# Kernel tuning notes

Hardware: AMD Instinct MI355X
Metric: run time of the kernel (lower is better)

## Reference

```python
import jax, jax.numpy as jnp
import numpy as np

V, H, I, E, K, L = 32000, 1024, 4096, 8, 2, 2
B, S = 1, 2048

def setup_inputs() -> dict:
    key = jax.random.key(0)
    ks = jax.random.split(key, 8)
    s = 0.02
    d = {}
    d["input_ids"] = jax.random.randint(ks[0], (B, S), 0, V)
    d["emb"] = jax.random.normal(ks[1], (V, H), jnp.float32) * s
    d["router_w"] = jax.random.normal(ks[2], (L, E, H), jnp.float32) * s
    d["router_b"] = jnp.zeros((L, E), jnp.float32)
    d["fc1_w"] = jax.random.normal(ks[3], (L, E, I, H), jnp.float32) * s
    d["fc1_b"] = jnp.zeros((L, E, I), jnp.float32)
    d["fc2_w"] = jax.random.normal(ks[4], (L, E, H, I), jnp.float32) * s
    d["fc2_b"] = jnp.zeros((L, E, H), jnp.float32)
    d["ln_g"] = jnp.ones((L, H), jnp.float32)
    d["ln_b"] = jnp.zeros((L, H), jnp.float32)
    d["head_w"] = jax.random.normal(ks[5], (V, H), jnp.float32) * s
    d["head_b"] = jnp.zeros((V,), jnp.float32)
    return d

def _moe_layer(h, rw, rb, f1w, f1b, f2w, f2b, g, b):
    # h: [T,H]
    T = h.shape[0]
    logits = h @ rw.T + rb                                  # [T,E]
    top_w, sel = jax.lax.top_k(logits, K)                   # [T,K]
    top_w = jax.nn.softmax(top_w, axis=-1)
    sel_oh = sel[None, :, :] == jnp.arange(E)[:, None, None]  # [E,T,K]
    mask = sel_oh.any(-1)                                     # [E,T]
    w_tok = jnp.sum(jnp.where(sel_oh, top_w[None], 0.0), -1)  # [E,T]
    cnt = mask.sum(-1).astype(h.dtype)                        # [E]
    # faithful to source: per-expert SCALAR weight = mean of routing weights of routed tokens
    scal = jnp.where(cnt > 0, w_tok.sum(-1) / jnp.maximum(cnt, 1.0), 0.0)  # [E]
    a = jax.nn.gelu(jnp.einsum('th,eih->eti', h, f1w) + f1b[:, None, :], approximate=False)
    eo = jnp.einsum('eti,ehi->eth', a, f2w) + f2b[:, None, :]             # [E,T,H]
    out = jnp.einsum('et,eth->th', mask.astype(h.dtype) * scal[:, None], eo)
    mu = out.mean(-1, keepdims=True)
    var = out.var(-1, keepdims=True)
    out = (out - mu) / jnp.sqrt(var + 1e-5) * g + b
    counts = sel_oh.sum((1, 2)).astype(h.dtype)
    aux = jnp.mean((counts - T / E) ** 2) * 0.01
    return out, aux

def reference(input_ids, emb, router_w, router_b, fc1_w, fc1_b, fc2_w, fc2_b, ln_g, ln_b, head_w, head_b):
    h = emb[input_ids].reshape(-1, H)   # [T,H]
    aux_total = jnp.float32(0.0)
    for l in range(L):
        h, aux = _moe_layer(h, router_w[l], router_b[l], fc1_w[l], fc1_b[l],
                            fc2_w[l], fc2_b[l], ln_g[l], ln_b[l])
        aux_total = aux_total + aux
    logits = h @ head_w.T + head_b
    return logits.reshape(B, S, V), aux_total
```

## Files before the change

kernel.cpp:

```cpp
#include <hip/hip_runtime.h>
#include <math.h>

constexpr int kT = 2048;
constexpr int kH = 1024;
constexpr int kI = 4096;
constexpr int kE = 8;
constexpr int kV = 32000;
constexpr int kL = 2;
constexpr int kR = 4096;
constexpr int kSK = 4;
constexpr int kNB = kR / 128 + kE - 1;

typedef __attribute__((ext_vector_type(4))) float f32x4;
typedef __attribute__((ext_vector_type(8))) short bf16x8;

__device__ inline unsigned cvtpk(float lo, float hi) {
  unsigned r;
  asm("v_cvt_pk_bf16_f32 %0, %1, %2" : "=v"(r) : "v"(lo), "v"(hi));
  return r;
}

__device__ inline unsigned short f2bf(float x) {
  union { float f; unsigned u; } c; c.f = x;
  unsigned u = c.u;
  u += 0x7FFFu + ((u >> 16) & 1u);
  return (unsigned short)(u >> 16);
}

__device__ inline void dec2(float x, float y,
                            unsigned& p1, unsigned& p2, unsigned& p3) {
  unsigned ux = __float_as_uint(x), uy = __float_as_uint(y);
  unsigned x1 = ux & 0xFFFF0000u, y1 = uy & 0xFFFF0000u;
  float rx = x - __uint_as_float(x1), ry = y - __uint_as_float(y1);
  unsigned x2 = __float_as_uint(rx) & 0xFFFF0000u;
  unsigned y2 = __float_as_uint(ry) & 0xFFFF0000u;
  float sx = rx - __uint_as_float(x2), sy = ry - __uint_as_float(y2);
  p1 = (x1 >> 16) | y1;
  p2 = (x2 >> 16) | y2;
  p3 = (__float_as_uint(sx) >> 16) | (__float_as_uint(sy) & 0xFFFF0000u);
}

__device__ inline int swz(int e) { return e ^ (((e >> 6) & 3) << 3); }


__global__ void gather_k(const int* __restrict__ ids, const float* __restrict__ emb,
                         float* __restrict__ h) {
  int t = blockIdx.x;
  int id = ids[t];
  const float4* src = (const float4*)(emb + (size_t)id * kH);
  float4* dst = (float4*)(h + (size_t)t * kH);
  dst[threadIdx.x] = src[threadIdx.x];
}

__global__ void router_k(const float* __restrict__ h, const float* __restrict__ rw,
                         const float* __restrict__ rb, float* __restrict__ logits) {
  int t = blockIdx.x;
  int lg = threadIdx.x & 31;
  int e = threadIdx.x >> 5;
  const float* hr = h + (size_t)t * kH;
  const float* wr = rw + (size_t)e * kH;
  float p = 0.f;
  for (int k = lg * 4; k < kH; k += 128) {
    float4 a = *(const float4*)(hr + k);
    float4 b = *(const float4*)(wr + k);
    p += a.x * b.x + a.y * b.y + a.z * b.z + a.w * b.w;
  }
  for (int o = 16; o > 0; o >>= 1) p += __shfl_down(p, o, 32);
  if (lg == 0) logits[t * kE + e] = p + rb[e];
}

__global__ void topk_k(const float* __restrict__ logits, int* __restrict__ sel,
                       float* __restrict__ w_sum, int* __restrict__ cnt) {
  int t = blockIdx.x * blockDim.x + threadIdx.x;
  if (t >= kT) return;
  float v[8];
#pragma unroll
  for (int e = 0; e < 8; e++) v[e] = logits[t * 8 + e];
  int e1 = 0; float v1 = v[0];
#pragma unroll
  for (int e = 1; e < 8; e++) if (v[e] > v1) { v1 = v[e]; e1 = e; }
  int e2 = -1; float v2 = -3.4e38f;
#pragma unroll
  for (int e = 0; e < 8; e++) if (e != e1 && v[e] > v2) { v2 = v[e]; e2 = e; }
  float z = expf(v2 - v1);
  float w1 = 1.f / (1.f + z);
  float w2 = z * w1;
  sel[t * 2] = e1;
  sel[t * 2 + 1] = e2;
  atomicAdd(&w_sum[e1], w1);
  atomicAdd(&w_sum[e2], w2);
  atomicAdd(&cnt[e1], 1);
  atomicAdd(&cnt[e2], 1);
}

__global__ void finalize_k(const int* __restrict__ cnt, const float* __restrict__ w_sum,
                           float* __restrict__ scal, int* __restrict__ off,
                           int* __restrict__ fill, float* __restrict__ aux,
                           int* __restrict__ blk_e, int* __restrict__ blk_m) {
  if (threadIdx.x == 0) {
    int o = 0;
    float a = 0.f;
    for (int e = 0; e < 8; e++) {
      off[e] = o;
      o += cnt[e];
      fill[e] = 0;
      int c = cnt[e];
      scal[e] = c > 0 ? w_sum[e] / (float)c : 0.f;
      float d = (float)c - 256.f;
      a += d * d;
    }
    aux[0] += 0.01f * (a * 0.125f);
    int nb = 0;
    for (int e = 0; e < 8; e++)
      for (int m = 0; m < cnt[e]; m += 128) { blk_e[nb] = e; blk_m[nb] = m; nb++; }
    for (int i = nb; i < kNB; i++) { blk_e[i] = -1; blk_m[i] = 0; }
  }
}

__global__ void scatter_k(const int* __restrict__ sel, const int* __restrict__ off,
                          int* __restrict__ fill, int* __restrict__ list,
                          int* __restrict__ pos) {
  int t = blockIdx.x * blockDim.x + threadIdx.x;
  if (t >= kT) return;
#pragma unroll
  for (int s = 0; s < 2; s++) {
    int e = sel[t * 2 + s];
    int p = atomicAdd(&fill[e], 1);
    int slot = off[e] + p;
    list[slot] = t;
    pos[t * 2 + s] = slot;
  }
}

__global__ void cvt_k(const float* __restrict__ src, unsigned short* __restrict__ dst, long n) {
  long i = ((long)blockIdx.x * 256 + threadIdx.x) * 8;
  if (i >= n) return;
  float4 a = *(const float4*)(src + i);
  float4 b = *(const float4*)(src + i + 4);
  uint4 pk;
  pk.x = (unsigned)f2bf(a.x) | ((unsigned)f2bf(a.y) << 16);
  pk.y = (unsigned)f2bf(a.z) | ((unsigned)f2bf(a.w) << 16);
  pk.z = (unsigned)f2bf(b.x) | ((unsigned)f2bf(b.y) << 16);
  pk.w = (unsigned)f2bf(b.z) | ((unsigned)f2bf(b.w) << 16);
  *(uint4*)(dst + i) = pk;
}

__global__ void combine_ln_k(const float* __restrict__ ccomp, const int* __restrict__ pos,
                             float* __restrict__ h, const float* __restrict__ g,
                             const float* __restrict__ b) {
  int t = blockIdx.x;
  int s0 = pos[t * 2], s1 = pos[t * 2 + 1];
  int k = threadIdx.x * 4;
  float4 v = {0.f, 0.f, 0.f, 0.f};
#pragma unroll
  for (int kc = 0; kc < kSK; kc++) {
    const float* base = ccomp + (size_t)kc * ((size_t)kR * kH);
    float4 a = *(const float4*)(base + (size_t)s0 * kH + k);
    float4 c = *(const float4*)(base + (size_t)s1 * kH + k);
    v.x += a.x + c.x; v.y += a.y + c.y; v.z += a.z + c.z; v.w += a.w + c.w;
  }
  float s = v.x + v.y + v.z + v.w;
  float sq = v.x * v.x + v.y * v.y + v.z * v.z + v.w * v.w;
  for (int o = 32; o > 0; o >>= 1) {
    s += __shfl_down(s, o);
    sq += __shfl_down(sq, o);
  }
  __shared__ float ss[4], sqs[4];
  int wave = threadIdx.x >> 6, lane = threadIdx.x & 63;
  if (lane == 0) { ss[wave] = s; sqs[wave] = sq; }
  __syncthreads();
  __shared__ float mu, inv;
  if (threadIdx.x == 0) {
    float st = ss[0] + ss[1] + ss[2] + ss[3];
    float sqt = sqs[0] + sqs[1] + sqs[2] + sqs[3];
    float m = st / (float)kH;
    float var = sqt / (float)kH - m * m;
    mu = m;
    inv = 1.f / sqrtf(var + 1e-5f);
  }
  __syncthreads();
  float4 gg = *(const float4*)(g + k);
  float4 bb = *(const float4*)(b + k);
  float4 o;
  o.x = (v.x - mu) * inv * gg.x + bb.x;
  o.y = (v.y - mu) * inv * gg.y + bb.y;
  o.z = (v.z - mu) * inv * gg.z + bb.z;
  o.w = (v.w - mu) * inv * gg.w + bb.w;
  *(float4*)(h + (size_t)t * kH + k) = o;
}

__global__ void aux_write_k(float* __restrict__ out, const float* __restrict__ aux) {
  out[(size_t)kT * kV] = aux[0];
}

template <int MODE>
__launch_bounds__(256)
__global__ void tgemm_k(const float* __restrict__ Abase, int ldA,
                        const float* __restrict__ Bbase,
                        const float* __restrict__ bias,
                        float* __restrict__ Cout,
                        const int* __restrict__ list,
                        const int* __restrict__ off,
                        const int* __restrict__ cnt,
                        const float* __restrict__ scal,
                        const int* __restrict__ blk_e,
                        const int* __restrict__ blk_m,
                        int N, int Kd) {
  const int e = blk_e[blockIdx.x];
  if (e < 0) return;
  const int m0 = blk_m[blockIdx.x];
  const int M = cnt[e];
  int nb = blockIdx.y, kc = 0;
  if constexpr (MODE == 1) { nb = blockIdx.y >> 2; kc = blockIdx.y & 3; }
  const int n0 = nb * 128;
  const int roff = off[e];
  const float* Bp = Bbase + (size_t)e * (size_t)N * (size_t)Kd;
  const float* be = bias + (size_t)e * (size_t)N;
  const int kBeg = (MODE == 1) ? kc * (Kd >> 2) : 0;
  const int kEnd = (MODE == 1) ? kBeg + (Kd >> 2) : Kd;

  __shared__ __align__(16) unsigned short As[3][128 * 32];
  __shared__ __align__(16) unsigned short Bs[3][128 * 32];

  const int tid = threadIdx.x, w = tid >> 6, l = tid & 63;

  const int srow = tid >> 1, scolh = (tid & 1) * 16;
  int gr = m0 + srow; if (gr > M - 1) gr = M - 1;
  long arow;
  if constexpr (MODE == 0) arow = list[roff + gr];
  else arow = roff + gr;
  const float* asrc = Abase + arow * (long)ldA + scolh;
  const float* bsrc = Bp + (size_t)(n0 + srow) * (size_t)Kd + scolh;
  const int e0 = srow * 32 + scolh;
  const int s0 = swz(e0), s1 = swz(e0 + 8);

  f32x4 acc[4][4] = {};
  const int wm = w >> 1, wn = w & 1;
  const int fr = l & 15, fk = (l >> 4) * 8;

  float4 rva[4], rvb[4];
  unsigned qa1[8], qa2[8], qa3[8], qb1[8], qb2[8], qb3[8];

#define LOADT(K0)                                   \
  _Pragma("unroll") for (int i = 0; i < 4; i++) {   \
    rva[i] = *(const float4*)(asrc + (K0) + i * 4); \
    rvb[i] = *(const float4*)(bsrc + (K0) + i * 4); \
  }

#define DECALL()                                               \
  {                                                            \
    float xa[16], xb[16];                                      \
    *(float4*)&xa[0] = rva[0]; *(float4*)&xa[4] = rva[1];      \
    *(float4*)&xa[8] = rva[2]; *(float4*)&xa[12] = rva[3];     \
    *(float4*)&xb[0] = rvb[0]; *(float4*)&xb[4] = rvb[1];      \
    *(float4*)&xb[8] = rvb[2]; *(float4*)&xb[12] = rvb[3];     \
    _Pragma("unroll") for (int i = 0; i < 8; i++) {            \
      dec2(xa[2 * i], xa[2 * i + 1], qa1[i], qa2[i], qa3[i]);  \
      dec2(xb[2 * i], xb[2 * i + 1], qb1[i], qb2[i], qb3[i]);  \
    }                                                          \
  }

  LOADT(kBeg);
  DECALL();

  for (int k0 = kBeg; k0 < kEnd; k0 += 32) {
    *(uint4*)&As[0][s0] = *(uint4*)&qa1[0]; *(uint4*)&As[0][s1] = *(uint4*)&qa1[4];
    *(uint4*)&As[1][s0] = *(uint4*)&qa2[0]; *(uint4*)&As[1][s1] = *(uint4*)&qa2[4];
    *(uint4*)&As[2][s0] = *(uint4*)&qa3[0]; *(uint4*)&As[2][s1] = *(uint4*)&qa3[4];
    *(uint4*)&Bs[0][s0] = *(uint4*)&qb1[0]; *(uint4*)&Bs[0][s1] = *(uint4*)&qb1[4];
    *(uint4*)&Bs[1][s0] = *(uint4*)&qb2[0]; *(uint4*)&Bs[1][s1] = *(uint4*)&qb2[4];
    *(uint4*)&Bs[2][s0] = *(uint4*)&qb3[0]; *(uint4*)&Bs[2][s1] = *(uint4*)&qb3[4];
    __syncthreads();
    const bool more = (k0 + 32 < kEnd);
    if (more) LOADT(k0 + 32);

    bf16x8 bf1[4], bf2[4], bf3[4];
#pragma unroll
    for (int bn = 0; bn < 4; bn++) {
      int se = swz((wn * 64 + bn * 16 + fr) * 32 + fk);
      bf1[bn] = *(const bf16x8*)(&Bs[0][se]);
      bf2[bn] = *(const bf16x8*)(&Bs[1][se]);
      bf3[bn] = *(const bf16x8*)(&Bs[2][se]);
    }
#pragma unroll
    for (int am = 0; am < 4; am++) {
      int se = swz((wm * 64 + am * 16 + fr) * 32 + fk);
      bf16x8 a1 = *(const bf16x8*)(&As[0][se]);
      bf16x8 a2 = *(const bf16x8*)(&As[1][se]);
      bf16x8 a3 = *(const bf16x8*)(&As[2][se]);
#pragma unroll
      for (int bn = 0; bn < 4; bn++) {
        f32x4 c = acc[am][bn];
        c = __builtin_amdgcn_mfma_f32_16x16x32_bf16(a3, bf1[bn], c, 0, 0, 0);
        c = __builtin_amdgcn_mfma_f32_16x16x32_bf16(a2, bf2[bn], c, 0, 0, 0);
        c = __builtin_amdgcn_mfma_f32_16x16x32_bf16(a1, bf3[bn], c, 0, 0, 0);
        c = __builtin_amdgcn_mfma_f32_16x16x32_bf16(a2, bf1[bn], c, 0, 0, 0);
        c = __builtin_amdgcn_mfma_f32_16x16x32_bf16(a1, bf2[bn], c, 0, 0, 0);
        c = __builtin_amdgcn_mfma_f32_16x16x32_bf16(a1, bf1[bn], c, 0, 0, 0);
        acc[am][bn] = c;
      }
    }
    if (more) DECALL();
    __syncthreads();
  }
#undef LOADT
#undef DECALL

  const int r0 = (l >> 4) * 4, cc = l & 15;
#pragma unroll
  for (int am = 0; am < 4; am++) {
#pragma unroll
    for (int bn = 0; bn < 4; bn++) {
      int gn = n0 + wn * 64 + bn * 16 + cc;
      float bv;
      if constexpr (MODE == 1) bv = (kc == 0) ? be[gn] : 0.f;
      else bv = be[gn];
#pragma unroll
      for (int j = 0; j < 4; j++) {
        int gm = m0 + wm * 64 + am * 16 + r0 + j;
        if (gm >= M) continue;
        float v = acc[am][bn][j] + bv;
        if constexpr (MODE == 0) {
          float g = 0.5f * v * (1.f + erff(v * 0.70710678118654752f));
          Cout[(size_t)(roff + gm) * (size_t)N + gn] = g;
        } else {
          Cout[(size_t)kc * ((size_t)kR * kH) + (size_t)(roff + gm) * (size_t)N + gn] =
              scal[e] * v;
        }
      }
    }
  }
}

template <int MODE>
__launch_bounds__(256)
__global__ void wgemm_k(const unsigned short* __restrict__ Abase, int ldA,
                        const unsigned short* __restrict__ Bbase,
                        const float* __restrict__ bias,
                        float* __restrict__ Cout,
                        unsigned short* __restrict__ Cbf,
                        const int* __restrict__ list,
                        const int* __restrict__ off,
                        const int* __restrict__ cnt,
                        const float* __restrict__ scal,
                        const int* __restrict__ blk_e,
                        const int* __restrict__ blk_m,
                        int N, int Kd) {
  const int e = blk_e[blockIdx.x];
  if (e < 0) return;
  const int m0 = blk_m[blockIdx.x];
  const int M = cnt[e];
  int nb = blockIdx.y, kc = 0;
  if constexpr (MODE == 1) { nb = blockIdx.y >> 2; kc = blockIdx.y & 3; }
  const int n0 = nb * 128;
  const int roff = off[e];
  const unsigned short* Bp = Bbase + (size_t)e * (size_t)N * (size_t)Kd;
  const float* be = bias + (size_t)e * (size_t)N;
  const int kBeg = (MODE == 1) ? kc * (Kd >> 2) : 0;
  const int kEnd = (MODE == 1) ? kBeg + (Kd >> 2) : Kd;

  __shared__ __align__(16) unsigned short As[128 * 64];
  __shared__ __align__(16) unsigned short Bs[128 * 64];

  const int tid = threadIdx.x, w = tid >> 6, l = tid & 63;

  const unsigned short* asrc[4];
  const unsigned short* bsrc[4];
#pragma unroll
  for (int i = 0; i < 4; i++) {
    int r = w * 8 + i * 32 + (l >> 3);
    int gr = m0 + r; if (gr > M - 1) gr = M - 1;
    long grow;
    if constexpr (MODE == 0) grow = list[roff + gr];
    else grow = roff + gr;
    asrc[i] = Abase + grow * (long)ldA + (l & 7) * 8;
    bsrc[i] = Bp + (size_t)(n0 + r) * (size_t)Kd + (l & 7) * 8;
  }

  f32x4 acc[4][4] = {};
  const int wm = w >> 1, wn = w & 1;
  const int fr = l & 15, fk = (l >> 4) * 8;

  for (int k0 = kBeg; k0 < kEnd; k0 += 64) {
#pragma unroll
    for (int i = 0; i < 4; i++) {
      __builtin_amdgcn_global_load_lds(
          (const __attribute__((address_space(1))) unsigned int*)(const void*)(asrc[i] + k0),
          (__attribute__((address_space(3))) unsigned int*)(void*)(As + w * 512 + i * 2048),
          16, 0, 0);
      __builtin_amdgcn_global_load_lds(
          (const __attribute__((address_space(1))) unsigned int*)(const void*)(bsrc[i] + k0),
          (__attribute__((address_space(3))) unsigned int*)(void*)(Bs + w * 512 + i * 2048),
          16, 0, 0);
    }
    __syncthreads();
#pragma unroll
    for (int ks = 0; ks < 2; ks++) {
      bf16x8 af[4], bfr[4];
#pragma unroll
      for (int am = 0; am < 4; am++)
        af[am] = *(const bf16x8*)(As + (wm * 64 + am * 16 + fr) * 64 + ks * 32 + fk);
#pragma unroll
      for (int bn = 0; bn < 4; bn++)
        bfr[bn] = *(const bf16x8*)(Bs + (wn * 64 + bn * 16 + fr) * 64 + ks * 32 + fk);
#pragma unroll
      for (int am = 0; am < 4; am++)
#pragma unroll
        for (int bn = 0; bn < 4; bn++)
          acc[am][bn] = __builtin_amdgcn_mfma_f32_16x16x32_bf16(af[am], bfr[bn], acc[am][bn], 0, 0, 0);
    }
    __syncthreads();
  }

  const int r0 = (l >> 4) * 4, cc = l & 15;
#pragma unroll
  for (int am = 0; am < 4; am++) {
#pragma unroll
    for (int bn = 0; bn < 4; bn++) {
      int gn = n0 + wn * 64 + bn * 16 + cc;
      float bv;
      if constexpr (MODE == 1) bv = (kc == 0) ? be[gn] : 0.f;
      else bv = be[gn];
#pragma unroll
      for (int j = 0; j < 4; j++) {
        int gm = m0 + wm * 64 + am * 16 + r0 + j;
        if (gm >= M) continue;
        float v = acc[am][bn][j] + bv;
        if constexpr (MODE == 0) {
          float g = 0.5f * v * (1.f + erff(v * 0.70710678118654752f));
          Cbf[(size_t)(roff + gm) * (size_t)N + gn] = f2bf(g);
        } else {
          Cout[(size_t)kc * ((size_t)kR * kH) + (size_t)(roff + gm) * (size_t)N + gn] =
              scal[e] * v;
        }
      }
    }
  }
}

__launch_bounds__(256)
__global__ void hgemm_k(const unsigned short* __restrict__ hbf,
                        const float* __restrict__ Bw,
                        const float* __restrict__ bias,
                        float* __restrict__ Cout) {
  int bx = blockIdx.x, by = blockIdx.y;
  {
    int lin = by * gridDim.x + bx;
    int nwg = gridDim.x * gridDim.y;
    int q = nwg >> 3, r = nwg & 7;
    int xcd = lin & 7, idx = lin >> 3;
    int swzb = (xcd < r ? xcd * (q + 1) : r * (q + 1) + (xcd - r) * q) + idx;
    bx = swzb % gridDim.x;
    by = swzb / gridDim.x;
  }
  const int m0 = bx * 128;
  const int n0 = by * 128;

  __shared__ __align__(16) unsigned short As[128 * 64];
  __shared__ __align__(16) unsigned short Bs[128 * 64];

  const int tid = threadIdx.x, w = tid >> 6, l = tid & 63;

  const unsigned short* asrc[4];
  const float* bsrc[4];
#pragma unroll
  for (int i = 0; i < 4; i++) {
    int r = w * 8 + i * 32 + (l >> 3);
    asrc[i] = hbf + (size_t)(m0 + r) * kH + (l & 7) * 8;
    bsrc[i] = Bw + (size_t)(n0 + r) * kH + (l & 7) * 8;
  }
  const int ldstB = w * 512 + (l >> 3) * 64 + (((l & 7) ^ (l >> 3)) * 8);

  f32x4 acc[4][4] = {};
  const int wm = w >> 1, wn = w & 1;
  const int fr = l & 15, fk = (l >> 4) * 8;
  const int col0 = (((l >> 4) + 0) ^ (l & 7)) * 8;
  const int col1 = (((l >> 4) + 4) ^ (l & 7)) * 8;

  float4 rb[4][2];
#define LOADB(K0)                                            \
  _Pragma("unroll") for (int i = 0; i < 4; i++) {            \
    rb[i][0] = *(const float4*)(bsrc[i] + (K0));             \
    rb[i][1] = *(const float4*)(bsrc[i] + (K0) + 4);         \
  }

  LOADB(0);

  for (int k0 = 0; k0 < kH; k0 += 64) {
#pragma unroll
    for (int i = 0; i < 4; i++) {
      __builtin_amdgcn_global_load_lds(
          (const __attribute__((address_space(1))) unsigned int*)(const void*)(asrc[i] + k0),
          (__attribute__((address_space(3))) unsigned int*)(void*)(As + w * 512 + i * 2048),
          16, 0, 0);
      uint4 pb;
      pb.x = cvtpk(rb[i][0].x, rb[i][0].y);
      pb.y = cvtpk(rb[i][0].z, rb[i][0].w);
      pb.z = cvtpk(rb[i][1].x, rb[i][1].y);
      pb.w = cvtpk(rb[i][1].z, rb[i][1].w);
      *(uint4*)(Bs + ldstB + i * 2048) = pb;
    }
    __syncthreads();
    if (k0 + 64 < kH) LOADB(k0 + 64);
#pragma unroll
    for (int ks = 0; ks < 2; ks++) {
      const int ck = ks ? col1 : col0;
      bf16x8 af[4], bfr[4];
#pragma unroll
      for (int am = 0; am < 4; am++)
        af[am] = *(const bf16x8*)(As + (wm * 64 + am * 16 + fr) * 64 + ks * 32 + fk);
#pragma unroll
      for (int bn = 0; bn < 4; bn++)
        bfr[bn] = *(const bf16x8*)(Bs + (wn * 64 + bn * 16 + fr) * 64 + ck);
#pragma unroll
      for (int am = 0; am < 4; am++)
#pragma unroll
        for (int bn = 0; bn < 4; bn++)
          acc[am][bn] = __builtin_amdgcn_mfma_f32_16x16x32_bf16(af[am], bfr[bn], acc[am][bn], 0, 0, 0);
    }
    __syncthreads();
  }
#undef LOADB

  const int r0 = (l >> 4) * 4, cc = l & 15;
#pragma unroll
  for (int am = 0; am < 4; am++) {
#pragma unroll
    for (int bn = 0; bn < 4; bn++) {
      int gn = n0 + wn * 64 + bn * 16 + cc;
      float bv = bias[gn];
#pragma unroll
      for (int j = 0; j < 4; j++) {
        int gm = m0 + wm * 64 + am * 16 + r0 + j;
        Cout[(size_t)gm * (size_t)kV + gn] = acc[am][bn][j] + bv;
      }
    }
  }
}


extern "C" void kernel_launch(void* const* d_in, const int* in_sizes, int n_in,
                              void* d_out, int out_size, void* d_ws, size_t ws_size,
                              hipStream_t stream) {
  (void)in_sizes; (void)n_in; (void)out_size; (void)ws_size;
  const int* ids = (const int*)d_in[0];
  const float* emb = (const float*)d_in[1];
  const float* router_w = (const float*)d_in[2];
  const float* router_b = (const float*)d_in[3];
  const float* fc1_w = (const float*)d_in[4];
  const float* fc1_b = (const float*)d_in[5];
  const float* fc2_w = (const float*)d_in[6];
  const float* fc2_b = (const float*)d_in[7];
  const float* ln_g = (const float*)d_in[8];
  const float* ln_b = (const float*)d_in[9];
  const float* head_w = (const float*)d_in[10];
  const float* head_b = (const float*)d_in[11];
  float* out = (float*)d_out;

  float* ws_f = (float*)d_ws;
  float* h       = ws_f;
  float* logits  = h + (size_t)kT * kH;
  float* w_sum   = logits + (size_t)kT * kE;
  float* scal    = w_sum + kE;
  float* aux     = scal + kE;
  int* sel  = (int*)(aux + 1);
  int* cnt  = sel + 2 * kT;
  int* off  = cnt + kE;
  int* fill = off + kE;
  int* list = fill + kE;
  int* pos  = list + kR;
  int* blk_e = pos + 2 * kT;
  int* blk_m = blk_e + kNB;
  unsigned short* h_bf = (unsigned short*)(blk_m + kNB);

  float* a_f32  = out;
  float* c_comp = a_f32 + (size_t)kR * kI;
  unsigned short* a_bf = (unsigned short*)out;
  unsigned short* wbf  = (unsigned short*)(c_comp + (size_t)kSK * kR * kH);

  hipMemsetAsync(aux, 0, sizeof(float), stream);
  gather_k<<<kT, 256, 0, stream>>>(ids, emb, h);

  for (int l = 0; l < kL; l++) {
    hipMemsetAsync(w_sum, 0, kE * sizeof(float), stream);
    hipMemsetAsync(cnt, 0, kE * sizeof(int), stream);
    router_k<<<kT, 256, 0, stream>>>(h, router_w + (size_t)l * kE * kH,
                                     router_b + (size_t)l * kE, logits);
    topk_k<<<kT / 256, 256, 0, stream>>>(logits, sel, w_sum, cnt);
    finalize_k<<<1, 64, 0, stream>>>(cnt, w_sum, scal, off, fill, aux, blk_e, blk_m);
    scatter_k<<<kT / 256, 256, 0, stream>>>(sel, off, fill, list, pos);

    if (l == 0) {
      tgemm_k<0><<<dim3(kNB, kI / 128), 256, 0, stream>>>(
          h, kH, fc1_w + (size_t)l * kE * kI * kH, fc1_b + (size_t)l * kE * kI,
          a_f32, list, off, cnt, scal, blk_e, blk_m, kI, kH);
      tgemm_k<1><<<dim3(kNB, (kH / 128) * kSK), 256, 0, stream>>>(
          a_f32, kI, fc2_w + (size_t)l * kE * kH * kI, fc2_b + (size_t)l * kE * kH,
          c_comp, list, off, cnt, scal, blk_e, blk_m, kH, kI);
    } else {
      cvt_k<<<(int)(((long)kT * kH) / 2048), 256, 0, stream>>>(h, h_bf, (long)kT * kH);
      cvt_k<<<(int)(((long)kE * kI * kH) / 2048), 256, 0, stream>>>(
          fc1_w + (size_t)l * kE * kI * kH, wbf, (long)kE * kI * kH);
      wgemm_k<0><<<dim3(kNB, kI / 128), 256, 0, stream>>>(
          h_bf, kH, wbf, fc1_b + (size_t)l * kE * kI,
          nullptr, a_bf, list, off, cnt, scal, blk_e, blk_m, kI, kH);
      cvt_k<<<(int)(((long)kE * kH * kI) / 2048), 256, 0, stream>>>(
          fc2_w + (size_t)l * kE * kH * kI, wbf, (long)kE * kH * kI);
      wgemm_k<1><<<dim3(kNB, (kH / 128) * kSK), 256, 0, stream>>>(
          a_bf, kI, wbf, fc2_b + (size_t)l * kE * kH,
          c_comp, nullptr, list, off, cnt, scal, blk_e, blk_m, kH, kI);
    }

    combine_ln_k<<<kT, 256, 0, stream>>>(c_comp, pos, h,
                                         ln_g + (size_t)l * kH, ln_b + (size_t)l * kH);
  }

  cvt_k<<<(int)(((long)kT * kH) / 2048), 256, 0, stream>>>(h, h_bf, (long)kT * kH);
  hgemm_k<<<dim3(kT / 128, kV / 128), 256, 0, stream>>>(h_bf, head_w, head_b, out);

  aux_write_k<<<1, 1, 0, stream>>>(out, aux);
}
```

Before: 1.354 ms.

## Pre-split layer-0 activations into bf16x3 planes and load A via global_load_lds

For layer 0, gathered token activations are pre-decomposed into three bf16 planes in a swizzled, 128-padded layout by a new kernel. The fc1 GEMM now writes its GELU output directly as three swizzled bf16 planes. Both split-precision GEMMs then stream the A operand straight into LDS with global_load_lds instead of loading fp32, decomposing in registers and storing to LDS. This removes per-block redundant A decomposition and the register and VALU cost of the old path. In exchange it adds an extra pre-pass kernel, more output stores in fc1's epilogue, padded buffers and a list memset.

```diff
diff --git a/kernel.cpp b/kernel.cpp
--- a/kernel.cpp
+++ b/kernel.cpp
@@ -8,6 +8,7 @@
 constexpr int kV = 32000;
 constexpr int kL = 2;
 constexpr int kR = 4096;
+constexpr int kRp = 5120;
 constexpr int kSK = 4;
 constexpr int kNB = kR / 128 + kE - 1;
 
@@ -38,6 +39,18 @@
   p1 = (x1 >> 16) | y1;
   p2 = (x2 >> 16) | y2;
   p3 = (__float_as_uint(sx) >> 16) | (__float_as_uint(sy) & 0xFFFF0000u);
+}
+
+__device__ inline void dec1(float x, unsigned short& b1, unsigned short& b2,
+                            unsigned short& b3) {
+  unsigned u = __float_as_uint(x);
+  unsigned x1 = u & 0xFFFF0000u;
+  float r = x - __uint_as_float(x1);
+  unsigned x2 = __float_as_uint(r) & 0xFFFF0000u;
+  float s = r - __uint_as_float(x2);
+  b1 = (unsigned short)(x1 >> 16);
+  b2 = (unsigned short)(x2 >> 16);
+  b3 = (unsigned short)(__float_as_uint(s) >> 16);
 }
 
 __device__ inline int swz(int e) { return e ^ (((e >> 6) & 3) << 3); }
@@ -102,7 +115,7 @@
     float a = 0.f;
     for (int e = 0; e < 8; e++) {
       off[e] = o;
-      o += cnt[e];
+      o += (cnt[e] + 127) & ~127;
       fill[e] = 0;
       int c = cnt[e];
       scal[e] = c > 0 ? w_sum[e] / (float)c : 0.f;
@@ -145,6 +158,27 @@
   *(uint4*)(dst + i) = pk;
 }
 
+__global__ void hdec_k(const float* __restrict__ h, const int* __restrict__ list,
+                       unsigned short* __restrict__ hp, long PH) {
+  int s = blockIdx.x * 2 + (threadIdx.x >> 7);
+  int k8 = (threadIdx.x & 127) * 8;
+  int t = list[s];
+  const float* src = h + (size_t)t * kH + k8;
+  float4 a = *(const float4*)(src);
+  float4 b = *(const float4*)(src + 4);
+  float x[8];
+  *(float4*)&x[0] = a; *(float4*)&x[4] = b;
+  unsigned q1[4], q2[4], q3[4];
+#pragma unroll
+  for (int i = 0; i < 4; i++) dec2(x[2 * i], x[2 * i + 1], q1[i], q2[i], q3[i]);
+  int sw = (s >> 2) & 3;
+  int colp = (k8 & ~31) | ((((k8 >> 3) & 3) ^ sw) << 3);
+  long base = (long)s * kH + colp;
+  *(uint4*)(hp + 0 * PH + base) = *(uint4*)q1;
+  *(uint4*)(hp + 1 * PH + base) = *(uint4*)q2;
+  *(uint4*)(hp + 2 * PH + base) = *(uint4*)q3;
+}
+
 __global__ void combine_ln_k(const float* __restrict__ ccomp, const int* __restrict__ pos,
                              float* __restrict__ h, const float* __restrict__ g,
                              const float* __restrict__ b) {
@@ -154,7 +188,7 @@
   float4 v = {0.f, 0.f, 0.f, 0.f};
 #pragma unroll
   for (int kc = 0; kc < kSK; kc++) {
-    const float* base = ccomp + (size_t)kc * ((size_t)kR * kH);
+    const float* base = ccomp + (size_t)kc * ((size_t)kRp * kH);
     float4 a = *(const float4*)(base + (size_t)s0 * kH + k);
     float4 c = *(const float4*)(base + (size_t)s1 * kH + k);
     v.x += a.x + c.x; v.y += a.y + c.y; v.z += a.z + c.z; v.w += a.w + c.w;
@@ -195,11 +229,11 @@
 
 template <int MODE>
 __launch_bounds__(256)
-__global__ void tgemm_k(const float* __restrict__ Abase, int ldA,
+__global__ void tgemm_k(const unsigned short* __restrict__ Ap, long PA, int ldA,
                         const float* __restrict__ Bbase,
                         const float* __restrict__ bias,
                         float* __restrict__ Cout,
-                        const int* __restrict__ list,
+                        unsigned short* __restrict__ Cp, long PCp,
                         const int* __restrict__ off,
                         const int* __restrict__ cnt,
                         const float* __restrict__ scal,
@@ -219,75 +253,82 @@
   const int kBeg = (MODE == 1) ? kc * (Kd >> 2) : 0;
   const int kEnd = (MODE == 1) ? kBeg + (Kd >> 2) : Kd;
 
-  __shared__ __align__(16) unsigned short As[3][128 * 32];
-  __shared__ __align__(16) unsigned short Bs[3][128 * 32];
+  __shared__ __align__(16) unsigned short AsL[3][128 * 32];
+  __shared__ __align__(16) unsigned short BsL[3][128 * 32];
 
   const int tid = threadIdx.x, w = tid >> 6, l = tid & 63;
 
+  long abase[2];
+#pragma unroll
+  for (int i = 0; i < 2; i++) {
+    int r = w * 16 + i * 64 + (l >> 2);
+    int gr = m0 + r; if (gr > M - 1) gr = M - 1;
+    abase[i] = (long)(roff + gr) * ldA + (l & 3) * 8;
+  }
+
   const int srow = tid >> 1, scolh = (tid & 1) * 16;
-  int gr = m0 + srow; if (gr > M - 1) gr = M - 1;
-  long arow;
-  if constexpr (MODE == 0) arow = list[roff + gr];
-  else arow = roff + gr;
-  const float* asrc = Abase + arow * (long)ldA + scolh;
   const float* bsrc = Bp + (size_t)(n0 + srow) * (size_t)Kd + scolh;
   const int e0 = srow * 32 + scolh;
-  const int s0 = swz(e0), s1 = swz(e0 + 8);
+  const int s0b = swz(e0), s1b = swz(e0 + 8);
 
   f32x4 acc[4][4] = {};
   const int wm = w >> 1, wn = w & 1;
   const int fr = l & 15, fk = (l >> 4) * 8;
-
-  float4 rva[4], rvb[4];
-  unsigned qa1[8], qa2[8], qa3[8], qb1[8], qb2[8], qb3[8];
-
-#define LOADT(K0)                                   \
-  _Pragma("unroll") for (int i = 0; i < 4; i++) {   \
-    rva[i] = *(const float4*)(asrc + (K0) + i * 4); \
-    rvb[i] = *(const float4*)(bsrc + (K0) + i * 4); \
-  }
-
-#define DECALL()                                               \
+  const int cola = ((l >> 4) ^ ((fr >> 2) & 3)) * 8;
+
+  float4 rvb[4];
+  unsigned qb1[8], qb2[8], qb3[8];
+
+#define LOADB(K0)                                      \
+  _Pragma("unroll") for (int i = 0; i < 4; i++)        \
+    rvb[i] = *(const float4*)(bsrc + (K0) + i * 4);
+
+#define DECB()                                                 \
   {                                                            \
-    float xa[16], xb[16];                                      \
-    *(float4*)&xa[0] = rva[0]; *(float4*)&xa[4] = rva[1];      \
-    *(float4*)&xa[8] = rva[2]; *(float4*)&xa[12] = rva[3];     \
+    float xb[16];                                              \
     *(float4*)&xb[0] = rvb[0]; *(float4*)&xb[4] = rvb[1];      \
     *(float4*)&xb[8] = rvb[2]; *(float4*)&xb[12] = rvb[3];     \
-    _Pragma("unroll") for (int i = 0; i < 8; i++) {            \
-      dec2(xa[2 * i], xa[2 * i + 1], qa1[i], qa2[i], qa3[i]);  \
+    _Pragma("unroll") for (int i = 0; i < 8; i++)              \
       dec2(xb[2 * i], xb[2 * i + 1], qb1[i], qb2[i], qb3[i]);  \
-    }                                                          \
-  }
-
-  LOADT(kBeg);
-  DECALL();
+  }
+
+  LOADB(kBeg);
+  DECB();
 
   for (int k0 = kBeg; k0 < kEnd; k0 += 32) {
-    *(uint4*)&As[0][s0] = *(uint4*)&qa1[0]; *(uint4*)&As[0][s1] = *(uint4*)&qa1[4];
-    *(uint4*)&As[1][s0] = *(uint4*)&qa2[0]; *(uint4*)&As[1][s1] = *(uint4*)&qa2[4];
-    *(uint4*)&As[2][s0] = *(uint4*)&qa3[0]; *(uint4*)&As[2][s1] = *(uint4*)&qa3[4];
-    *(uint4*)&Bs[0][s0] = *(uint4*)&qb1[0]; *(uint4*)&Bs[0][s1] = *(uint4*)&qb1[4];
-    *(uint4*)&Bs[1][s0] = *(uint4*)&qb2[0]; *(uint4*)&Bs[1][s1] = *(uint4*)&qb2[4];
-    *(uint4*)&Bs[2][s0] = *(uint4*)&qb3[0]; *(uint4*)&Bs[2][s1] = *(uint4*)&qb3[4];
+#pragma unroll
+    for (int p = 0; p < 3; p++) {
+#pragma unroll
+      for (int i = 0; i < 2; i++) {
+        __builtin_amdgcn_global_load_lds(
+            (const __attribute__((address_space(1))) unsigned int*)(const void*)
+                (Ap + (long)p * PA + abase[i] + k0),
+            (__attribute__((address_space(3))) unsigned int*)(void*)
+                (&AsL[p][(w * 16 + i * 64) * 32]),
+            16, 0, 0);
+      }
+    }
+    *(uint4*)&BsL[0][s0b] = *(uint4*)&qb1[0]; *(uint4*)&BsL[0][s1b] = *(uint4*)&qb1[4];
+    *(uint4*)&BsL[1][s0b] = *(uint4*)&qb2[0]; *(uint4*)&BsL[1][s1b] = *(uint4*)&qb2[4];
+    *(uint4*)&BsL[2][s0b] = *(uint4*)&qb3[0]; *(uint4*)&BsL[2][s1b] = *(uint4*)&qb3[4];
     __syncthreads();
     const bool more = (k0 + 32 < kEnd);
-    if (more) LOADT(k0 + 32);
+    if (more) LOADB(k0 + 32);
 
     bf16x8 bf1[4], bf2[4], bf3[4];
 #pragma unroll
     for (int bn = 0; bn < 4; bn++) {
       int se = swz((wn * 64 + bn * 16 + fr) * 32 + fk);
-      bf1[bn] = *(const bf16x8*)(&Bs[0][se]);
-      bf2[bn] = *(const bf16x8*)(&Bs[1][se]);
-      bf3[bn] = *(const bf16x8*)(&Bs[2][se]);
+      bf1[bn] = *(const bf16x8*)(&BsL[0][se]);
+      bf2[bn] = *(const bf16x8*)(&BsL[1][se]);
+      bf3[bn] = *(const bf16x8*)(&BsL[2][se]);
     }
 #pragma unroll
     for (int am = 0; am < 4; am++) {
-      int se = swz((wm * 64 + am * 16 + fr) * 32 + fk);
-      bf16x8 a1 = *(const bf16x8*)(&As[0][se]);
-      bf16x8 a2 = *(const bf16x8*)(&As[1][se]);
-      bf16x8 a3 = *(const bf16x8*)(&As[2][se]);
+      int ra = (wm * 64 + am * 16 + fr) * 32 + cola;
+      bf16x8 a1 = *(const bf16x8*)(&AsL[0][ra]);
+      bf16x8 a2 = *(const bf16x8*)(&AsL[1][ra]);
+      bf16x8 a3 = *(const bf16x8*)(&AsL[2][ra]);
 #pragma unroll
       for (int bn = 0; bn < 4; bn++) {
         f32x4 c = acc[am][bn];
@@ -300,13 +341,14 @@
         acc[am][bn] = c;
       }
     }
-    if (more) DECALL();
+    if (more) DECB();
     __syncthreads();
   }
-#undef LOADT
-#undef DECALL
+#undef LOADB
+#undef DECB
 
   const int r0 = (l >> 4) * 4, cc = l & 15;
+  const int swp = l >> 4;
 #pragma unroll
   for (int am = 0; am < 4; am++) {
 #pragma unroll
@@ -315,6 +357,9 @@
       float bv;
       if constexpr (MODE == 1) bv = (kc == 0) ? be[gn] : 0.f;
       else bv = be[gn];
+      int colp = 0;
+      if constexpr (MODE == 0)
+        colp = (gn & ~31) | ((((gn >> 3) & 3) ^ swp) << 3) | (gn & 7);
 #pragma unroll
       for (int j = 0; j < 4; j++) {
         int gm = m0 + wm * 64 + am * 16 + r0 + j;
@@ -322,9 +367,14 @@
         float v = acc[am][bn][j] + bv;
         if constexpr (MODE == 0) {
           float g = 0.5f * v * (1.f + erff(v * 0.70710678118654752f));
-          Cout[(size_t)(roff + gm) * (size_t)N + gn] = g;
+          unsigned short b1, b2, b3;
+          dec1(g, b1, b2, b3);
+          long base = (long)(roff + gm) * N + colp;
+          Cp[0 * PCp + base] = b1;
+          Cp[1 * PCp + base] = b2;
+          Cp[2 * PCp + base] = b3;
         } else {
-          Cout[(size_t)kc * ((size_t)kR * kH) + (size_t)(roff + gm) * (size_t)N + gn] =
+          Cout[(size_t)kc * ((size_t)kRp * kH) + (size_t)(roff + gm) * (size_t)N + gn] =
               scal[e] * v;
         }
       }
@@ -430,7 +480,7 @@
           float g = 0.5f * v * (1.f + erff(v * 0.70710678118654752f));
           Cbf[(size_t)(roff + gm) * (size_t)N + gn] = f2bf(g);
         } else {
-          Cout[(size_t)kc * ((size_t)kR * kH) + (size_t)(roff + gm) * (size_t)N + gn] =
+          Cout[(size_t)kc * ((size_t)kRp * kH) + (size_t)(roff + gm) * (size_t)N + gn] =
               scal[e] * v;
         }
       }
@@ -568,15 +618,18 @@
   int* off  = cnt + kE;
   int* fill = off + kE;
   int* list = fill + kE;
-  int* pos  = list + kR;
+  int* pos  = list + kRp;
   int* blk_e = pos + 2 * kT;
   int* blk_m = blk_e + kNB;
   unsigned short* h_bf = (unsigned short*)(blk_m + kNB);
 
-  float* a_f32  = out;
-  float* c_comp = a_f32 + (size_t)kR * kI;
+  const long PA_h = (long)kRp * kH;
+  const long PA_a = (long)kRp * kI;
+  unsigned short* ap = (unsigned short*)out;
+  unsigned short* hp = ap + 3 * PA_a;
+  float* c_comp = (float*)(hp + 3 * PA_h);
   unsigned short* a_bf = (unsigned short*)out;
-  unsigned short* wbf  = (unsigned short*)(c_comp + (size_t)kSK * kR * kH);
+  unsigned short* wbf = a_bf + (size_t)kRp * kI;
 
   hipMemsetAsync(aux, 0, sizeof(float), stream);
   gather_k<<<kT, 256, 0, stream>>>(ids, emb, h);
@@ -584,6 +637,7 @@
   for (int l = 0; l < kL; l++) {
     hipMemsetAsync(w_sum, 0, kE * sizeof(float), stream);
     hipMemsetAsync(cnt, 0, kE * sizeof(int), stream);
+    hipMemsetAsync(list, 0, kRp * sizeof(int), stream);
     router_k<<<kT, 256, 0, stream>>>(h, router_w + (size_t)l * kE * kH,
                                      router_b + (size_t)l * kE, logits);
     topk_k<<<kT / 256, 256, 0, stream>>>(logits, sel, w_sum, cnt);
@@ -591,12 +645,13 @@
     scatter_k<<<kT / 256, 256, 0, stream>>>(sel, off, fill, list, pos);
 
     if (l == 0) {
+      hdec_k<<<kRp / 2, 256, 0, stream>>>(h, list, hp, PA_h);
       tgemm_k<0><<<dim3(kNB, kI / 128), 256, 0, stream>>>(
-          h, kH, fc1_w + (size_t)l * kE * kI * kH, fc1_b + (size_t)l * kE * kI,
-          a_f32, list, off, cnt, scal, blk_e, blk_m, kI, kH);
+          hp, PA_h, kH, fc1_w + (size_t)l * kE * kI * kH, fc1_b + (size_t)l * kE * kI,
+          nullptr, ap, PA_a, off, cnt, scal, blk_e, blk_m, kI, kH);
       tgemm_k<1><<<dim3(kNB, (kH / 128) * kSK), 256, 0, stream>>>(
-          a_f32, kI, fc2_w + (size_t)l * kE * kH * kI, fc2_b + (size_t)l * kE * kH,
-          c_comp, list, off, cnt, scal, blk_e, blk_m, kH, kI);
+          ap, PA_a, kI, fc2_w + (size_t)l * kE * kH * kI, fc2_b + (size_t)l * kE * kH,
+          c_comp, nullptr, 0, off, cnt, scal, blk_e, blk_m, kH, kI);
     } else {
       cvt_k<<<(int)(((long)kT * kH) / 2048), 256, 0, stream>>>(h, h_bf, (long)kT * kH);
       cvt_k<<<(int)(((long)kE * kI * kH) / 2048), 256, 0, stream>>>(
```

Result: slower. 1.402 ms (+3.6%).

## Fuse fp32-to-bf16 weight conversion into expert GEMM loads and LN output

Applied to the files above, without the earlier changes.

Drops the separate cvt kernels for the fc1/fc2 weights. The layer-1 expert GEMM now loads fp32 weights into registers, converts them with packed bf16 instructions, and stores them into a swizzled LDS tile, with the next tile's loads issued before the MMA loop. The combine+layernorm kernel also writes the bf16 copy of h directly, removing the h conversions. Expert row offsets are padded to multiples of 128 and the buffers grow to match. This saves a full write and read of 64M bf16 weights per layer, at the cost of reading fp32 weights inside the GEMM (redundantly across M-blocks) and using more registers.

```diff
diff --git a/kernel.cpp b/kernel.cpp
--- a/kernel.cpp
+++ b/kernel.cpp
@@ -8,6 +8,7 @@
 constexpr int kV = 32000;
 constexpr int kL = 2;
 constexpr int kR = 4096;
+constexpr int kRp = 5120;
 constexpr int kSK = 4;
 constexpr int kNB = kR / 128 + kE - 1;
 
@@ -102,7 +103,7 @@
     float a = 0.f;
     for (int e = 0; e < 8; e++) {
       off[e] = o;
-      o += cnt[e];
+      o += (cnt[e] + 127) & ~127;
       fill[e] = 0;
       int c = cnt[e];
       scal[e] = c > 0 ? w_sum[e] / (float)c : 0.f;
@@ -132,29 +133,16 @@
   }
 }
 
-__global__ void cvt_k(const float* __restrict__ src, unsigned short* __restrict__ dst, long n) {
-  long i = ((long)blockIdx.x * 256 + threadIdx.x) * 8;
-  if (i >= n) return;
-  float4 a = *(const float4*)(src + i);
-  float4 b = *(const float4*)(src + i + 4);
-  uint4 pk;
-  pk.x = (unsigned)f2bf(a.x) | ((unsigned)f2bf(a.y) << 16);
-  pk.y = (unsigned)f2bf(a.z) | ((unsigned)f2bf(a.w) << 16);
-  pk.z = (unsigned)f2bf(b.x) | ((unsigned)f2bf(b.y) << 16);
-  pk.w = (unsigned)f2bf(b.z) | ((unsigned)f2bf(b.w) << 16);
-  *(uint4*)(dst + i) = pk;
-}
-
 __global__ void combine_ln_k(const float* __restrict__ ccomp, const int* __restrict__ pos,
-                             float* __restrict__ h, const float* __restrict__ g,
-                             const float* __restrict__ b) {
+                             float* __restrict__ h, unsigned short* __restrict__ hbf,
+                             const float* __restrict__ g, const float* __restrict__ b) {
   int t = blockIdx.x;
   int s0 = pos[t * 2], s1 = pos[t * 2 + 1];
   int k = threadIdx.x * 4;
   float4 v = {0.f, 0.f, 0.f, 0.f};
 #pragma unroll
   for (int kc = 0; kc < kSK; kc++) {
-    const float* base = ccomp + (size_t)kc * ((size_t)kR * kH);
+    const float* base = ccomp + (size_t)kc * ((size_t)kRp * kH);
     float4 a = *(const float4*)(base + (size_t)s0 * kH + k);
     float4 c = *(const float4*)(base + (size_t)s1 * kH + k);
     v.x += a.x + c.x; v.y += a.y + c.y; v.z += a.z + c.z; v.w += a.w + c.w;
@@ -187,6 +175,10 @@
   o.z = (v.z - mu) * inv * gg.z + bb.z;
   o.w = (v.w - mu) * inv * gg.w + bb.w;
   *(float4*)(h + (size_t)t * kH + k) = o;
+  uint2 pk;
+  pk.x = (unsigned)f2bf(o.x) | ((unsigned)f2bf(o.y) << 16);
+  pk.y = (unsigned)f2bf(o.z) | ((unsigned)f2bf(o.w) << 16);
+  *(uint2*)(hbf + (size_t)t * kH + k) = pk;
 }
 
 __global__ void aux_write_k(float* __restrict__ out, const float* __restrict__ aux) {
@@ -324,7 +316,7 @@
           float g = 0.5f * v * (1.f + erff(v * 0.70710678118654752f));
           Cout[(size_t)(roff + gm) * (size_t)N + gn] = g;
         } else {
-          Cout[(size_t)kc * ((size_t)kR * kH) + (size_t)(roff + gm) * (size_t)N + gn] =
+          Cout[(size_t)kc * ((size_t)kRp * kH) + (size_t)(roff + gm) * (size_t)N + gn] =
               scal[e] * v;
         }
       }
@@ -334,18 +326,18 @@
 
 template <int MODE>
 __launch_bounds__(256)
-__global__ void wgemm_k(const unsigned short* __restrict__ Abase, int ldA,
-                        const unsigned short* __restrict__ Bbase,
-                        const float* __restrict__ bias,
-                        float* __restrict__ Cout,
-                        unsigned short* __restrict__ Cbf,
-                        const int* __restrict__ list,
-                        const int* __restrict__ off,
-                        const int* __restrict__ cnt,
-                        const float* __restrict__ scal,
-                        const int* __restrict__ blk_e,
-                        const int* __restrict__ blk_m,
-                        int N, int Kd) {
+__global__ void wfgemm_k(const unsigned short* __restrict__ Abase, int ldA,
+                         const float* __restrict__ Bbase,
+                         const float* __restrict__ bias,
+                         float* __restrict__ Cout,
+                         unsigned short* __restrict__ Cbf,
+                         const int* __restrict__ list,
+                         const int* __restrict__ off,
+                         const int* __restrict__ cnt,
+                         const float* __restrict__ scal,
+                         const int* __restrict__ blk_e,
+                         const int* __restrict__ blk_m,
+                         int N, int Kd) {
   const int e = blk_e[blockIdx.x];
   if (e < 0) return;
   const int m0 = blk_m[blockIdx.x];
@@ -354,7 +346,7 @@
   if constexpr (MODE == 1) { nb = blockIdx.y >> 2; kc = blockIdx.y & 3; }
   const int n0 = nb * 128;
   const int roff = off[e];
-  const unsigned short* Bp = Bbase + (size_t)e * (size_t)N * (size_t)Kd;
+  const float* Bp = Bbase + (size_t)e * (size_t)N * (size_t)Kd;
   const float* be = bias + (size_t)e * (size_t)N;
   const int kBeg = (MODE == 1) ? kc * (Kd >> 2) : 0;
   const int kEnd = (MODE == 1) ? kBeg + (Kd >> 2) : Kd;
@@ -365,7 +357,7 @@
   const int tid = threadIdx.x, w = tid >> 6, l = tid & 63;
 
   const unsigned short* asrc[4];
-  const unsigned short* bsrc[4];
+  const float* bsrc[4];
 #pragma unroll
   for (int i = 0; i < 4; i++) {
     int r = w * 8 + i * 32 + (l >> 3);
@@ -376,10 +368,22 @@
     asrc[i] = Abase + grow * (long)ldA + (l & 7) * 8;
     bsrc[i] = Bp + (size_t)(n0 + r) * (size_t)Kd + (l & 7) * 8;
   }
+  const int ldstB = w * 512 + (l >> 3) * 64 + (((l & 7) ^ (l >> 3)) * 8);
 
   f32x4 acc[4][4] = {};
   const int wm = w >> 1, wn = w & 1;
   const int fr = l & 15, fk = (l >> 4) * 8;
+  const int col0 = (((l >> 4) + 0) ^ (l & 7)) * 8;
+  const int col1 = (((l >> 4) + 4) ^ (l & 7)) * 8;
+
+  float4 rb[4][2];
+#define LOADB(K0)                                            \
+  _Pragma("unroll") for (int i = 0; i < 4; i++) {            \
+    rb[i][0] = *(const float4*)(bsrc[i] + (K0));             \
+    rb[i][1] = *(const float4*)(bsrc[i] + (K0) + 4);         \
+  }
+
+  LOADB(kBeg);
 
   for (int k0 = kBeg; k0 < kEnd; k0 += 64) {
 #pragma unroll
@@ -388,21 +392,25 @@
           (const __attribute__((address_space(1))) unsigned int*)(const void*)(asrc[i] + k0),
           (__attribute__((address_space(3))) unsigned int*)(void*)(As + w * 512 + i * 2048),
           16, 0, 0);
-      __builtin_amdgcn_global_load_lds(
-          (const __attribute__((address_space(1))) unsigned int*)(const void*)(bsrc[i] + k0),
-          (__attribute__((address_space(3))) unsigned int*)(void*)(Bs + w * 512 + i * 2048),
-          16, 0, 0);
+      uint4 pb;
+      pb.x = cvtpk(rb[i][0].x, rb[i][0].y);
+      pb.y = cvtpk(rb[i][0].z, rb[i][0].w);
+      pb.z = cvtpk(rb[i][1].x, rb[i][1].y);
+      pb.w = cvtpk(rb[i][1].z, rb[i][1].w);
+      *(uint4*)(Bs + ldstB + i * 2048) = pb;
     }
     __syncthreads();
+    if (k0 + 64 < kEnd) LOADB(k0 + 64);
 #pragma unroll
     for (int ks = 0; ks < 2; ks++) {
+      const int ck = ks ? col1 : col0;
       bf16x8 af[4], bfr[4];
 #pragma unroll
       for (int am = 0; am < 4; am++)
         af[am] = *(const bf16x8*)(As + (wm * 64 + am * 16 + fr) * 64 + ks * 32 + fk);
 #pragma unroll
       for (int bn = 0; bn < 4; bn++)
-        bfr[bn] = *(const bf16x8*)(Bs + (wn * 64 + bn * 16 + fr) * 64 + ks * 32 + fk);
+        bfr[bn] = *(const bf16x8*)(Bs + (wn * 64 + bn * 16 + fr) * 64 + ck);
 #pragma unroll
       for (int am = 0; am < 4; am++)
 #pragma unroll
@@ -411,6 +419,7 @@
     }
     __syncthreads();
   }
+#undef LOADB
 
   const int r0 = (l >> 4) * 4, cc = l & 15;
 #pragma unroll
@@ -430,7 +439,7 @@
           float g = 0.5f * v * (1.f + erff(v * 0.70710678118654752f));
           Cbf[(size_t)(roff + gm) * (size_t)N + gn] = f2bf(g);
         } else {
-          Cout[(size_t)kc * ((size_t)kR * kH) + (size_t)(roff + gm) * (size_t)N + gn] =
+          Cout[(size_t)kc * ((size_t)kRp * kH) + (size_t)(roff + gm) * (size_t)N + gn] =
               scal[e] * v;
         }
       }
@@ -568,15 +577,14 @@
   int* off  = cnt + kE;
   int* fill = off + kE;
   int* list = fill + kE;
-  int* pos  = list + kR;
+  int* pos  = list + kRp;
   int* blk_e = pos + 2 * kT;
   int* blk_m = blk_e + kNB;
   unsigned short* h_bf = (unsigned short*)(blk_m + kNB);
 
   float* a_f32  = out;
-  float* c_comp = a_f32 + (size_t)kR * kI;
+  float* c_comp = a_f32 + (size_t)kRp * kI;
   unsigned short* a_bf = (unsigned short*)out;
-  unsigned short* wbf  = (unsigned short*)(c_comp + (size_t)kSK * kR * kH);
 
   hipMemsetAsync(aux, 0, sizeof(float), stream);
   gather_k<<<kT, 256, 0, stream>>>(ids, emb, h);
@@ -598,24 +606,18 @@
           a_f32, kI, fc2_w + (size_t)l * kE * kH * kI, fc2_b + (size_t)l * kE * kH,
           c_comp, list, off, cnt, scal, blk_e, blk_m, kH, kI);
     } else {
-      cvt_k<<<(int)(((long)kT * kH) / 2048), 256, 0, stream>>>(h, h_bf, (long)kT * kH);
-      cvt_k<<<(int)(((long)kE * kI * kH) / 2048), 256, 0, stream>>>(
-          fc1_w + (size_t)l * kE * kI * kH, wbf, (long)kE * kI * kH);
-      wgemm_k<0><<<dim3(kNB, kI / 128), 256, 0, stream>>>(
-          h_bf, kH, wbf, fc1_b + (size_t)l * kE * kI,
+      wfgemm_k<0><<<dim3(kNB, kI / 128), 256, 0, stream>>>(
+          h_bf, kH, fc1_w + (size_t)l * kE * kI * kH, fc1_b + (size_t)l * kE * kI,
           nullptr, a_bf, list, off, cnt, scal, blk_e, blk_m, kI, kH);
-      cvt_k<<<(int)(((long)kE * kH * kI) / 2048), 256, 0, stream>>>(
-          fc2_w + (size_t)l * kE * kH * kI, wbf, (long)kE * kH * kI);
-      wgemm_k<1><<<dim3(kNB, (kH / 128) * kSK), 256, 0, stream>>>(
-          a_bf, kI, wbf, fc2_b + (size_t)l * kE * kH,
+      wfgemm_k<1><<<dim3(kNB, (kH / 128) * kSK), 256, 0, stream>>>(
+          a_bf, kI, fc2_w + (size_t)l * kE * kH * kI, fc2_b + (size_t)l * kE * kH,
           c_comp, nullptr, list, off, cnt, scal, blk_e, blk_m, kH, kI);
     }
 
-    combine_ln_k<<<kT, 256, 0, stream>>>(c_comp, pos, h,
+    combine_ln_k<<<kT, 256, 0, stream>>>(c_comp, pos, h, h_bf,
                                          ln_g + (size_t)l * kH, ln_b + (size_t)l * kH);
   }
 
-  cvt_k<<<(int)(((long)kT * kH) / 2048), 256, 0, stream>>>(h, h_bf, (long)kT * kH);
   hgemm_k<<<dim3(kT / 128, kV / 128), 256, 0, stream>>>(h_bf, head_w, head_b, out);
 
   aux_write_k<<<1, 1, 0, stream>>>(out, aux);
```

New measurement: 1.325 ms. 1.02x faster.
